# Performance work log

Hardware: AMD Instinct MI355X
Metric: run time of the kernel (lower is better)

Reference implementation:

```python
import jax, jax.numpy as jnp
import numpy as np

B, N, D, H = 4, 2048, 256, 8
d = D // H          # 32 per-head dim
EPS = 1e-5
SCALE = 1.0 / float(np.sqrt(d))


def setup_inputs() -> dict:
    key = jax.random.key(0)
    ks = jax.random.split(key, 6)
    s = 0.02
    x = jax.random.normal(ks[0], (B, N, D), jnp.float32)
    # RoPE frequencies: theta_j = 10000^(-2j/d), angle = pos * theta
    inv_freq = 1.0 / (10000.0 ** (jnp.arange(0, d, 2, dtype=jnp.float32) / d))  # (d/2,)
    ang = jnp.arange(N, dtype=jnp.float32)[:, None] * inv_freq[None, :]          # (N, d/2)
    return {
        "x": x,
        "freqs_cos": jnp.cos(ang),
        "freqs_sin": jnp.sin(ang),
        "w_qkv": jax.random.normal(ks[1], (D, 3 * D), jnp.float32) * s,
        "b_qkv": jnp.zeros((3 * D,), jnp.float32),
        "w_proj": jax.random.normal(ks[2], (D, D), jnp.float32) * s,
        "b_proj": jnp.zeros((D,), jnp.float32),
        "ln1_g": jnp.ones((D,), jnp.float32),
        "ln1_b": jnp.zeros((D,), jnp.float32),
        "ln2_g": jnp.ones((D,), jnp.float32),
        "ln2_b": jnp.zeros((D,), jnp.float32),
        "w1": jax.random.normal(ks[3], (D, 2 * D), jnp.float32) * s,
        "b1": jnp.zeros((2 * D,), jnp.float32),
        "w2": jax.random.normal(ks[4], (2 * D, D), jnp.float32) * s,
        "b2": jnp.zeros((D,), jnp.float32),
    }


def _layer_norm(x, g, b):
    mu = jnp.mean(x, axis=-1, keepdims=True)
    var = jnp.mean(jnp.square(x - mu), axis=-1, keepdims=True)
    return (x - mu) * jax.lax.rsqrt(var + EPS) * g + b


def _rope(t, cos, sin):
    # t: (B,H,N,d); interleaved (even,odd) pairs viewed as complex, multiplied by e^{i*ang}
    tr = t.reshape(B, H, N, d // 2, 2)
    te, to = tr[..., 0], tr[..., 1]
    c = cos[None, None, :, :]
    s = sin[None, None, :, :]
    oe = te * c - to * s
    oo = te * s + to * c
    return jnp.stack([oe, oo], axis=-1).reshape(B, H, N, d)


def reference(x, freqs_cos, freqs_sin, w_qkv, b_qkv, w_proj, b_proj,
              ln1_g, ln1_b, ln2_g, ln2_b, w1, b1, w2, b2):
    # Pre-LN MHSA with RoPE (dropout = identity at eval)
    h = _layer_norm(x, ln1_g, ln1_b)
    qkv = (h @ w_qkv + b_qkv).reshape(B, N, 3, H, d).transpose(0, 2, 3, 1, 4)  # (B,3,H,N,d)
    q, k, v = qkv[:, 0], qkv[:, 1], qkv[:, 2]
    q = _rope(q, freqs_cos, freqs_sin)
    k = _rope(k, freqs_cos, freqs_sin)
    attn = jax.nn.softmax(jnp.einsum('bhnd,bhmd->bhnm', q, k) * SCALE, axis=-1)
    out = jnp.einsum('bhnm,bhmd->bhnd', attn, v).transpose(0, 2, 1, 3).reshape(B, N, D)
    x = x + (out @ w_proj + b_proj)
    h = _layer_norm(x, ln2_g, ln2_b)
    ffn = jax.nn.relu(h @ w1 + b1) @ w2 + b2
    return x + ffn
```

## Files before the change

### kernel.cpp

```cpp
#include <hip/hip_runtime.h>
#include <hip/hip_bf16.h>
#include <math.h>

#define Bsz 4
#define Nseq 2048
#define Dm 256
#define Hh 8
#define Hd 32
#define EPS_ 1e-5f
#define SCALE_ 0.17677669529663687f
#define QSC_ (0.17677669529663687f * 1.4426950408889634f)

typedef __attribute__((ext_vector_type(8))) short short8;
typedef __attribute__((ext_vector_type(4))) short short4v;
typedef __attribute__((ext_vector_type(4))) float f32x4;
typedef __attribute__((ext_vector_type(16))) float f32x16;

__device__ __forceinline__ void gload16(const void* g, void* l) {
    __builtin_amdgcn_global_load_lds(
        (const __attribute__((address_space(1))) void*)g,
        (__attribute__((address_space(3))) void*)l, 16, 0, 0);
}

__device__ __forceinline__ short bf16s(float f) {
    __hip_bfloat16 h = __float2bfloat16(f);
    return *(short*)&h;
}

__device__ __forceinline__ int pkbf(float a, float b) {
    __hip_bfloat16 lo = __float2bfloat16(a), hi2 = __float2bfloat16(b);
    return (int)(((unsigned int)*(unsigned short*)&hi2 << 16) |
                 (unsigned int)*(unsigned short*)&lo);
}

union I4S8 { int i[4]; short8 s; };

__global__ __launch_bounds__(256) void ln_kernel(const float* __restrict__ x,
                                                 const float* __restrict__ g,
                                                 const float* __restrict__ b,
                                                 __hip_bfloat16* __restrict__ out) {
    int row  = blockIdx.x * 4 + (threadIdx.x >> 6);
    int lane = threadIdx.x & 63;
    const float* xr = x + (size_t)row * Dm;
    float4 v = *(const float4*)(xr + lane * 4);
    float s  = v.x + v.y + v.z + v.w;
    float ss = v.x * v.x + v.y * v.y + v.z * v.z + v.w * v.w;
    #pragma unroll
    for (int off = 32; off; off >>= 1) {
        s  += __shfl_xor(s, off);
        ss += __shfl_xor(ss, off);
    }
    float mu  = s * (1.0f / Dm);
    float var = ss * (1.0f / Dm) - mu * mu;
    float rs  = rsqrtf(var + EPS_);
    float4 gv = *(const float4*)(g + lane * 4);
    float4 bv = *(const float4*)(b + lane * 4);
    short4v o4 = { bf16s((v.x - mu) * rs * gv.x + bv.x),
                   bf16s((v.y - mu) * rs * gv.y + bv.y),
                   bf16s((v.z - mu) * rs * gv.z + bv.z),
                   bf16s((v.w - mu) * rs * gv.w + bv.w) };
    *(short4v*)(out + (size_t)row * Dm + lane * 4) = o4;
}

__global__ __launch_bounds__(256) void wconv_kernel(
    const float* __restrict__ s0, const float* __restrict__ s1,
    const float* __restrict__ s2, const float* __restrict__ s3,
    __hip_bfloat16* __restrict__ d0, __hip_bfloat16* __restrict__ d1,
    __hip_bfloat16* __restrict__ d2, __hip_bfloat16* __restrict__ d3) {
    __shared__ float t[32][33];
    int bid = blockIdx.x;
    const float* src; __hip_bfloat16* dst; int K, N, tb;
    if (bid < 192)      { src = s0; dst = d0; K = 256; N = 768; tb = bid; }
    else if (bid < 256) { src = s1; dst = d1; K = 256; N = 256; tb = bid - 192; }
    else if (bid < 384) { src = s2; dst = d2; K = 256; N = 512; tb = bid - 256; }
    else                { src = s3; dst = d3; K = 512; N = 256; tb = bid - 384; }
    int tn = N >> 5;
    int k0 = (tb / tn) * 32, n0 = (tb % tn) * 32;
    int c = threadIdx.x & 31, r0 = threadIdx.x >> 5;
    #pragma unroll
    for (int i = 0; i < 4; i++) {
        int r = r0 + i * 8;
        t[r][c] = src[(size_t)(k0 + r) * N + n0 + c];
    }
    __syncthreads();
    #pragma unroll
    for (int i = 0; i < 4; i++) {
        int n = r0 + i * 8;
        dst[(size_t)(n0 + n) * K + k0 + c] = __float2bfloat16(t[c][n]);
    }
}

template <int TM, int EPI>
__global__ __launch_bounds__(256) void mfma_gemm(const __hip_bfloat16* __restrict__ A,
                                                 const __hip_bfloat16* __restrict__ Wt,
                                                 const float* __restrict__ bias,
                                                 const float* __restrict__ res,
                                                 float* __restrict__ Cf,
                                                 __hip_bfloat16* __restrict__ Cb,
                                                 int M, int Nn, int K) {
    constexpr int MF = TM / 64;
    __shared__ __align__(16) __hip_bfloat16 As[TM * 32];
    __shared__ __align__(16) __hip_bfloat16 Bs[64 * 32];
    const int tid = threadIdx.x, w = tid >> 6, lane = tid & 63;
    const int lm = lane & 15, lq = lane >> 4;
    const int bm = blockIdx.y * TM, bn = blockIdx.x * 64;
    f32x4 acc[MF][4];
    #pragma unroll
    for (int i = 0; i < MF; i++)
        #pragma unroll
        for (int j = 0; j < 4; j++) acc[i][j] = (f32x4){0.f, 0.f, 0.f, 0.f};

    const int sw = (lq ^ (lm & 3)) * 8;
    for (int k0 = 0; k0 < K; k0 += 32) {
        #pragma unroll
        for (int p = 0; p < MF; p++) {
            int c = p * 256 + tid;
            int r = c >> 2, gk = ((c & 3) ^ (r & 3)) * 8;
            gload16(A + (size_t)(bm + r) * K + k0 + gk, As + (p * 256 + w * 64) * 8);
        }
        {
            int r = tid >> 2, gk = ((tid & 3) ^ (r & 3)) * 8;
            gload16(Wt + (size_t)(bn + r) * K + k0 + gk, Bs + w * 512);
        }
        __syncthreads();
        short8 a[MF];
        #pragma unroll
        for (int mf = 0; mf < MF; mf++)
            a[mf] = *(const short8*)&As[(w * (TM / 4) + mf * 16 + lm) * 32 + sw];
        #pragma unroll
        for (int nf = 0; nf < 4; nf++) {
            short8 bfr = *(const short8*)&Bs[(nf * 16 + lm) * 32 + sw];
            #pragma unroll
            for (int mf = 0; mf < MF; mf++)
                acc[mf][nf] = __builtin_amdgcn_mfma_f32_16x16x32_bf16(a[mf], bfr, acc[mf][nf], 0, 0, 0);
        }
        __syncthreads();
    }
    #pragma unroll
    for (int nf = 0; nf < 4; nf++) {
        int cg = bn + nf * 16 + lm;
        float bi = bias[cg];
        #pragma unroll
        for (int mf = 0; mf < MF; mf++) {
            #pragma unroll
            for (int r = 0; r < 4; r++) {
                int rg = bm + w * (TM / 4) + mf * 16 + lq * 4 + r;
                float v = acc[mf][nf][r] + bi;
                if (EPI == 1) {
                    v = fmaxf(v, 0.f);
                    Cb[(size_t)rg * Nn + cg] = __float2bfloat16(v);
                } else {
                    v += res[(size_t)rg * Nn + cg];
                    Cf[(size_t)rg * Nn + cg] = v;
                }
            }
        }
    }
}

__global__ __launch_bounds__(256) void qkv_mfma(const __hip_bfloat16* __restrict__ A,
                                                const __hip_bfloat16* __restrict__ Wt,
                                                const float* __restrict__ bias,
                                                const float* __restrict__ fcos,
                                                const float* __restrict__ fsin,
                                                __hip_bfloat16* __restrict__ qout,
                                                __hip_bfloat16* __restrict__ kout,
                                                __hip_bfloat16* __restrict__ vt) {
    const int K = 256, Nn = 768;
    __shared__ __align__(16) __hip_bfloat16 As[128 * 32];
    __shared__ __align__(16) __hip_bfloat16 Bs[64 * 32];
    const int tid = threadIdx.x, w = tid >> 6, lane = tid & 63;
    const int lm = lane & 15, lq = lane >> 4;
    const int bm = blockIdx.y * 128, bn = blockIdx.x * 64;
    f32x4 acc[2][4];
    #pragma unroll
    for (int i = 0; i < 2; i++)
        #pragma unroll
        for (int j = 0; j < 4; j++) acc[i][j] = (f32x4){0.f, 0.f, 0.f, 0.f};

    const int sw = (lq ^ (lm & 3)) * 8;
    for (int k0 = 0; k0 < K; k0 += 32) {
        #pragma unroll
        for (int p = 0; p < 2; p++) {
            int c = p * 256 + tid;
            int r = c >> 2, gk = ((c & 3) ^ (r & 3)) * 8;
            gload16(A + (size_t)(bm + r) * K + k0 + gk, As + (p * 256 + w * 64) * 8);
        }
        {
            int r = tid >> 2, gk = ((tid & 3) ^ (r & 3)) * 8;
            gload16(Wt + (size_t)(bn + r) * K + k0 + gk, Bs + w * 512);
        }
        __syncthreads();
        short8 a0 = *(const short8*)&As[(w * 32 + lm) * 32 + sw];
        short8 a1 = *(const short8*)&As[(w * 32 + 16 + lm) * 32 + sw];
        #pragma unroll
        for (int nf = 0; nf < 4; nf++) {
            short8 bfr = *(const short8*)&Bs[(nf * 16 + lm) * 32 + sw];
            acc[0][nf] = __builtin_amdgcn_mfma_f32_16x16x32_bf16(a0, bfr, acc[0][nf], 0, 0, 0);
            acc[1][nf] = __builtin_amdgcn_mfma_f32_16x16x32_bf16(a1, bfr, acc[1][nf], 0, 0, 0);
        }
        __syncthreads();
    }
    const int seg = bn >> 8;
    #pragma unroll
    for (int nf = 0; nf < 4; nf++) {
        int cg = bn + nf * 16 + lm;
        int hh = (cg & 255) >> 5;
        int dd = (nf & 1) * 16 + lm;
        int i0 = dd >> 1;
        float bi = bias[cg];
        #pragma unroll
        for (int mf = 0; mf < 2; mf++) {
            #pragma unroll
            for (int r = 0; r < 4; r++) {
                int rg = bm + w * 32 + mf * 16 + lq * 4 + r;
                int bb = rg >> 11, n = rg & (Nseq - 1);
                float v = acc[mf][nf][r] + bi;
                if (seg == 2) {
                    vt[(((size_t)(bb * Hh + hh)) * Hd + dd) * Nseq + n] = __float2bfloat16(v);
                } else {
                    float vp = __shfl_xor(v, 1);
                    float cs = fcos[n * 16 + i0], sn = fsin[n * 16 + i0];
                    float outv = (dd & 1) ? (vp * sn + v * cs) : (v * cs - vp * sn);
                    if (seg == 0) outv *= QSC_;
                    __hip_bfloat16* dst = (seg == 0) ? qout : kout;
                    dst[(((size_t)(bb * Hh + hh)) * Nseq + n) * Hd + dd] = __float2bfloat16(outv);
                }
            }
        }
    }
}

__global__ __launch_bounds__(256) void attn_mfma(const __hip_bfloat16* __restrict__ q,
                                                 const __hip_bfloat16* __restrict__ k,
                                                 const __hip_bfloat16* __restrict__ vt,
                                                 __hip_bfloat16* __restrict__ att) {
    __shared__ __align__(16) __hip_bfloat16 Qs[128 * 32];
    __shared__ __align__(16) __hip_bfloat16 Ks[2][32 * 64];
    __shared__ __align__(16) __hip_bfloat16 Vs[2][32 * 64];
    __shared__ float smS[4][32];
    const int tid = threadIdx.x, w = tid >> 6;
    const int lane = tid & 63, l31 = lane & 31, hi = lane >> 5;
    const int bh = blockIdx.y, qbase = blockIdx.x * 128;
    const __hip_bfloat16* qp = q + ((size_t)bh * Nseq + qbase) * Hd;
    const __hip_bfloat16* kp = k + (size_t)bh * Nseq * Hd;
    const __hip_bfloat16* vp = vt + (size_t)bh * Hd * Nseq;

    const int r8 = tid >> 3, s8 = tid & 7;
    #pragma unroll
    for (int p = 0; p < 2; p++) {
        int c = p * 256 + tid, r = c >> 2, sl = c & 3;
        gload16(qp + r * 32 + ((sl ^ (r & 3)) * 8), Qs + (p * 256 + w * 64) * 8);
    }
    gload16(kp + (2 * r8 + (s8 >> 2)) * 32 + (((s8 & 3) ^ (r8 & 3)) * 8), Ks[0] + w * 512);
    gload16(vp + (size_t)r8 * Nseq + ((s8 ^ (r8 & 7)) * 8), Vs[0] + w * 512);
    __syncthreads();

    const int qrow = w * 32 + l31;
    short8 qf0 = *(const short8*)&Qs[qrow * 32 + ((hi ^ (l31 & 3)) * 8)];
    short8 qf1 = *(const short8*)&Qs[qrow * 32 + (((2 + hi) ^ (l31 & 3)) * 8)];

    f32x16 O;
    #pragma unroll
    for (int i = 0; i < 16; i++) O[i] = 0.f;
    float sm = 0.f;

    for (int kt = 0; kt < Nseq / 64; kt++) {
        const int cur = kt & 1;
        if (kt + 1 < Nseq / 64) {
            gload16(kp + ((kt + 1) * 64 + 2 * r8 + (s8 >> 2)) * 32 + (((s8 & 3) ^ (r8 & 3)) * 8),
                    Ks[cur ^ 1] + w * 512);
            gload16(vp + (size_t)r8 * Nseq + (kt + 1) * 64 + ((s8 ^ (r8 & 7)) * 8),
                    Vs[cur ^ 1] + w * 512);
        }
        f32x16 St0, St1;
        #pragma unroll
        for (int i = 0; i < 16; i++) { St0[i] = 0.f; St1[i] = 0.f; }
        {
            int prow = l31 >> 1;
            int elb = prow * 64 + (l31 & 1) * 32;
            short8 kf0 = *(const short8*)&Ks[cur][elb + ((hi ^ (prow & 3)) * 8)];
            short8 kf1 = *(const short8*)&Ks[cur][elb + (((2 + hi) ^ (prow & 3)) * 8)];
            St0 = __builtin_amdgcn_mfma_f32_32x32x16_bf16(kf0, qf0, St0, 0, 0, 0);
            St0 = __builtin_amdgcn_mfma_f32_32x32x16_bf16(kf1, qf1, St0, 0, 0, 0);
        }
        {
            int prow = 16 + (l31 >> 1);
            int elb = prow * 64 + (l31 & 1) * 32;
            short8 kf0 = *(const short8*)&Ks[cur][elb + ((hi ^ (prow & 3)) * 8)];
            short8 kf1 = *(const short8*)&Ks[cur][elb + (((2 + hi) ^ (prow & 3)) * 8)];
            St1 = __builtin_amdgcn_mfma_f32_32x32x16_bf16(kf0, qf0, St1, 0, 0, 0);
            St1 = __builtin_amdgcn_mfma_f32_32x32x16_bf16(kf1, qf1, St1, 0, 0, 0);
        }
        int pk0[8], pk1[8];
        #pragma unroll
        for (int p = 0; p < 8; p++) {
            float a = exp2f(St0[2 * p]), b = exp2f(St0[2 * p + 1]);
            sm += a + b;
            pk0[p] = pkbf(a, b);
        }
        #pragma unroll
        for (int p = 0; p < 8; p++) {
            float a = exp2f(St1[2 * p]), b = exp2f(St1[2 * p + 1]);
            sm += a + b;
            pk1[p] = pkbf(a, b);
        }
        #pragma unroll
        for (int t = 0; t < 4; t++) {
            const int* PK = (t >> 1) ? pk1 : pk0;
            const int base = 4 * (t & 1);
            int keep0 = hi ? PK[base + 2] : PK[base + 0];
            int keep1 = hi ? PK[base + 3] : PK[base + 1];
            int send0 = hi ? PK[base + 0] : PK[base + 2];
            int send1 = hi ? PK[base + 1] : PK[base + 3];
            int x0 = __shfl_xor(send0, 32);
            int x1 = __shfl_xor(send1, 32);
            I4S8 u;
            u.i[0] = hi ? x0 : keep0;
            u.i[1] = hi ? x1 : keep1;
            u.i[2] = hi ? keep0 : x0;
            u.i[3] = hi ? keep1 : x1;
            short8 vf = *(const short8*)&Vs[cur][l31 * 64 + (((2 * t + hi) ^ (l31 & 7)) * 8)];
            O = __builtin_amdgcn_mfma_f32_32x32x16_bf16(u.s, vf, O, 0, 0, 0);
        }
        __syncthreads();
    }
    sm += __shfl_xor(sm, 32);
    if (hi == 0) smS[w][l31] = sm;
    __syncthreads();
    const int bb = bh >> 3, hh = bh & 7;
    #pragma unroll
    for (int m = 0; m < 4; m++) {
        float4 sv = *(const float4*)&smS[w][8 * m + 4 * hi];
        #pragma unroll
        for (int i = 0; i < 4; i++) {
            int n = qbase + w * 32 + 8 * m + 4 * hi + i;
            att[((size_t)(bb * Nseq + n)) * Dm + hh * Hd + l31] =
                __float2bfloat16(O[4 * m + i] * (1.0f / sv[i]));
        }
    }
}

extern "C" void kernel_launch(void* const* d_in, const int* in_sizes, int n_in,
                              void* d_out, int out_size, void* d_ws, size_t ws_size,
                              hipStream_t stream) {
    const float* x      = (const float*)d_in[0];
    const float* fcos   = (const float*)d_in[1];
    const float* fsin   = (const float*)d_in[2];
    const float* w_qkv  = (const float*)d_in[3];
    const float* b_qkv  = (const float*)d_in[4];
    const float* w_proj = (const float*)d_in[5];
    const float* b_proj = (const float*)d_in[6];
    const float* ln1_g  = (const float*)d_in[7];
    const float* ln1_b  = (const float*)d_in[8];
    const float* ln2_g  = (const float*)d_in[9];
    const float* ln2_b  = (const float*)d_in[10];
    const float* w1     = (const float*)d_in[11];
    const float* b1     = (const float*)d_in[12];
    const float* w2     = (const float*)d_in[13];
    const float* b2     = (const float*)d_in[14];
    float* out = (float*)d_out;
    char* base = (char*)d_ws;
    const size_t MB = (size_t)1 << 20;

    __hip_bfloat16* h   = (__hip_bfloat16*)(base);
    __hip_bfloat16* qb  = (__hip_bfloat16*)(base + 4 * MB);
    __hip_bfloat16* kbf = (__hip_bfloat16*)(base + 8 * MB);
    __hip_bfloat16* vtb = (__hip_bfloat16*)(base + 12 * MB);
    __hip_bfloat16* att = (__hip_bfloat16*)(base + 16 * MB);
    float*          x2f = (float*)(base + 20 * MB);
    __hip_bfloat16* h2  = (__hip_bfloat16*)(base);
    __hip_bfloat16* ffn = (__hip_bfloat16*)(base + 28 * MB);
    __hip_bfloat16* wqT = (__hip_bfloat16*)(base + 40 * MB);
    __hip_bfloat16* wpT = (__hip_bfloat16*)(base + 40 * MB + 393216);
    __hip_bfloat16* w1T = (__hip_bfloat16*)(base + 40 * MB + 524288);
    __hip_bfloat16* w2T = (__hip_bfloat16*)(base + 40 * MB + 786432);

    const int rows = Bsz * Nseq;

    wconv_kernel<<<512, 256, 0, stream>>>(w_qkv, w_proj, w1, w2, wqT, wpT, w1T, w2T);
    ln_kernel<<<rows / 4, 256, 0, stream>>>(x, ln1_g, ln1_b, h);
    qkv_mfma<<<dim3(12, 64), 256, 0, stream>>>(h, wqT, b_qkv, fcos, fsin, qb, kbf, vtb);
    attn_mfma<<<dim3(Nseq / 128, Bsz * Hh), 256, 0, stream>>>(qb, kbf, vtb, att);
    mfma_gemm<64, 2><<<dim3(4, 128), 256, 0, stream>>>(att, wpT, b_proj, x, x2f, nullptr,
                                                       rows, 256, 256);
    ln_kernel<<<rows / 4, 256, 0, stream>>>(x2f, ln2_g, ln2_b, h2);
    mfma_gemm<128, 1><<<dim3(8, 64), 256, 0, stream>>>(h2, w1T, b1, nullptr, nullptr, ffn,
                                                       rows, 512, 256);
    mfma_gemm<64, 2><<<dim3(4, 128), 256, 0, stream>>>(ffn, w2T, b2, x2f, out, nullptr,
                                                       rows, 256, 512);
}
```

Before: 205.0 us.

## Split attention key range across wave pairs and cheapen exp/bf16 packing

Result: faster. 184.5 us (-10.0%).

```diff
diff --git a/kernel.cpp b/kernel.cpp
--- a/kernel.cpp
+++ b/kernel.cpp
@@ -27,10 +27,11 @@
     return *(short*)&h;
 }
 
-__device__ __forceinline__ int pkbf(float a, float b) {
-    __hip_bfloat16 lo = __float2bfloat16(a), hi2 = __float2bfloat16(b);
-    return (int)(((unsigned int)*(unsigned short*)&hi2 << 16) |
-                 (unsigned int)*(unsigned short*)&lo);
+union FU { float f; unsigned u; };
+
+__device__ __forceinline__ int pk2bf(float a, float b) {
+    FU ua, ub; ua.f = a; ub.f = b;
+    return (int)__builtin_amdgcn_perm(ub.u, ua.u, 0x07060302u);
 }
 
 union I4S8 { int i[4]; short8 s; };
@@ -235,28 +236,37 @@
                                                  const __hip_bfloat16* __restrict__ k,
                                                  const __hip_bfloat16* __restrict__ vt,
                                                  __hip_bfloat16* __restrict__ att) {
-    __shared__ __align__(16) __hip_bfloat16 Qs[128 * 32];
-    __shared__ __align__(16) __hip_bfloat16 Ks[2][32 * 64];
-    __shared__ __align__(16) __hip_bfloat16 Vs[2][32 * 64];
-    __shared__ float smS[4][32];
-    const int tid = threadIdx.x, w = tid >> 6;
-    const int lane = tid & 63, l31 = lane & 31, hi = lane >> 5;
-    const int bh = blockIdx.y, qbase = blockIdx.x * 128;
+    __shared__ __align__(16) char smem[4096 + 16384 + 16384 + 512];
+    __hip_bfloat16* Qs  = (__hip_bfloat16*)smem;
+    __hip_bfloat16* KsB = (__hip_bfloat16*)(smem + 4096);
+    __hip_bfloat16* VsB = (__hip_bfloat16*)(smem + 20480);
+    float* RedO = (float*)(smem + 4096);
+    float* RedS = (float*)(smem + 4096 + 8192);
+    float* smS  = (float*)(smem + 4096 + 8192 + 256);
+
+    const int tid = threadIdx.x, w = tid >> 6, lane = tid & 63;
+    const int l31 = lane & 31, hi = lane >> 5;
+    const int wq = w >> 1, wk = w & 1;
+    const int bh = blockIdx.y, qbase = blockIdx.x * 64;
     const __hip_bfloat16* qp = q + ((size_t)bh * Nseq + qbase) * Hd;
     const __hip_bfloat16* kp = k + (size_t)bh * Nseq * Hd;
     const __hip_bfloat16* vp = vt + (size_t)bh * Hd * Nseq;
-
     const int r8 = tid >> 3, s8 = tid & 7;
-    #pragma unroll
-    for (int p = 0; p < 2; p++) {
-        int c = p * 256 + tid, r = c >> 2, sl = c & 3;
-        gload16(qp + r * 32 + ((sl ^ (r & 3)) * 8), Qs + (p * 256 + w * 64) * 8);
-    }
-    gload16(kp + (2 * r8 + (s8 >> 2)) * 32 + (((s8 & 3) ^ (r8 & 3)) * 8), Ks[0] + w * 512);
-    gload16(vp + (size_t)r8 * Nseq + ((s8 ^ (r8 & 7)) * 8), Vs[0] + w * 512);
+
+    {
+        int r = tid >> 2, sl = tid & 3;
+        gload16(qp + r * 32 + ((sl ^ (r & 3)) * 8), Qs + w * 512);
+    }
+    #pragma unroll
+    for (int par = 0; par < 2; par++) {
+        gload16(kp + (par * 64 + 2 * r8 + (s8 >> 2)) * 32 + (((s8 & 3) ^ (r8 & 3)) * 8),
+                KsB + par * 2048 + w * 512);
+        gload16(vp + (size_t)r8 * Nseq + par * 64 + ((s8 ^ (r8 & 7)) * 8),
+                VsB + par * 2048 + w * 512);
+    }
     __syncthreads();
 
-    const int qrow = w * 32 + l31;
+    const int qrow = wq * 32 + l31;
     short8 qf0 = *(const short8*)&Qs[qrow * 32 + ((hi ^ (l31 & 3)) * 8)];
     short8 qf1 = *(const short8*)&Qs[qrow * 32 + (((2 + hi) ^ (l31 & 3)) * 8)];
 
@@ -265,50 +275,56 @@
     for (int i = 0; i < 16; i++) O[i] = 0.f;
     float sm = 0.f;
 
-    for (int kt = 0; kt < Nseq / 64; kt++) {
-        const int cur = kt & 1;
-        if (kt + 1 < Nseq / 64) {
-            gload16(kp + ((kt + 1) * 64 + 2 * r8 + (s8 >> 2)) * 32 + (((s8 & 3) ^ (r8 & 3)) * 8),
-                    Ks[cur ^ 1] + w * 512);
-            gload16(vp + (size_t)r8 * Nseq + (kt + 1) * 64 + ((s8 ^ (r8 & 7)) * 8),
-                    Vs[cur ^ 1] + w * 512);
-        }
+    for (int t = 0; t < 16; t++) {
+        const int buf = t & 1;
+        if (t + 1 < 16) {
+            const int kb2 = (t + 1) * 128;
+            #pragma unroll
+            for (int par = 0; par < 2; par++) {
+                gload16(kp + (kb2 + par * 64 + 2 * r8 + (s8 >> 2)) * 32 + (((s8 & 3) ^ (r8 & 3)) * 8),
+                        KsB + ((buf ^ 1) * 2 + par) * 2048 + w * 512);
+                gload16(vp + (size_t)r8 * Nseq + kb2 + par * 64 + ((s8 ^ (r8 & 7)) * 8),
+                        VsB + ((buf ^ 1) * 2 + par) * 2048 + w * 512);
+            }
+        }
+        const __hip_bfloat16* Kc = KsB + (buf * 2 + wk) * 2048;
+        const __hip_bfloat16* Vc = VsB + (buf * 2 + wk) * 2048;
         f32x16 St0, St1;
         #pragma unroll
         for (int i = 0; i < 16; i++) { St0[i] = 0.f; St1[i] = 0.f; }
         {
-            int prow = l31 >> 1;
-            int elb = prow * 64 + (l31 & 1) * 32;
-            short8 kf0 = *(const short8*)&Ks[cur][elb + ((hi ^ (prow & 3)) * 8)];
-            short8 kf1 = *(const short8*)&Ks[cur][elb + (((2 + hi) ^ (prow & 3)) * 8)];
+            int pr = l31 >> 1, elb = pr * 64 + (l31 & 1) * 32;
+            short8 kf0 = *(const short8*)&Kc[elb + ((hi ^ (pr & 3)) * 8)];
+            short8 kf1 = *(const short8*)&Kc[elb + (((2 + hi) ^ (pr & 3)) * 8)];
             St0 = __builtin_amdgcn_mfma_f32_32x32x16_bf16(kf0, qf0, St0, 0, 0, 0);
             St0 = __builtin_amdgcn_mfma_f32_32x32x16_bf16(kf1, qf1, St0, 0, 0, 0);
         }
         {
-            int prow = 16 + (l31 >> 1);
-            int elb = prow * 64 + (l31 & 1) * 32;
-            short8 kf0 = *(const short8*)&Ks[cur][elb + ((hi ^ (prow & 3)) * 8)];
-            short8 kf1 = *(const short8*)&Ks[cur][elb + (((2 + hi) ^ (prow & 3)) * 8)];
+            int pr = 16 + (l31 >> 1), elb = pr * 64 + (l31 & 1) * 32;
+            short8 kf0 = *(const short8*)&Kc[elb + ((hi ^ (pr & 3)) * 8)];
+            short8 kf1 = *(const short8*)&Kc[elb + (((2 + hi) ^ (pr & 3)) * 8)];
             St1 = __builtin_amdgcn_mfma_f32_32x32x16_bf16(kf0, qf0, St1, 0, 0, 0);
             St1 = __builtin_amdgcn_mfma_f32_32x32x16_bf16(kf1, qf1, St1, 0, 0, 0);
         }
         int pk0[8], pk1[8];
         #pragma unroll
         for (int p = 0; p < 8; p++) {
-            float a = exp2f(St0[2 * p]), b = exp2f(St0[2 * p + 1]);
+            float a = __builtin_amdgcn_exp2f(St0[2 * p]);
+            float b = __builtin_amdgcn_exp2f(St0[2 * p + 1]);
             sm += a + b;
-            pk0[p] = pkbf(a, b);
+            pk0[p] = pk2bf(a, b);
         }
         #pragma unroll
         for (int p = 0; p < 8; p++) {
-            float a = exp2f(St1[2 * p]), b = exp2f(St1[2 * p + 1]);
+            float a = __builtin_amdgcn_exp2f(St1[2 * p]);
+            float b = __builtin_amdgcn_exp2f(St1[2 * p + 1]);
             sm += a + b;
-            pk1[p] = pkbf(a, b);
-        }
-        #pragma unroll
-        for (int t = 0; t < 4; t++) {
-            const int* PK = (t >> 1) ? pk1 : pk0;
-            const int base = 4 * (t & 1);
+            pk1[p] = pk2bf(a, b);
+        }
+        #pragma unroll
+        for (int tt = 0; tt < 4; tt++) {
+            const int* PK = (tt >> 1) ? pk1 : pk0;
+            const int base = 4 * (tt & 1);
             int keep0 = hi ? PK[base + 2] : PK[base + 0];
             int keep1 = hi ? PK[base + 3] : PK[base + 1];
             int send0 = hi ? PK[base + 0] : PK[base + 2];
@@ -320,23 +336,36 @@
             u.i[1] = hi ? x1 : keep1;
             u.i[2] = hi ? keep0 : x0;
             u.i[3] = hi ? keep1 : x1;
-            short8 vf = *(const short8*)&Vs[cur][l31 * 64 + (((2 * t + hi) ^ (l31 & 7)) * 8)];
+            short8 vf = *(const short8*)&Vc[l31 * 64 + (((2 * tt + hi) ^ (l31 & 7)) * 8)];
             O = __builtin_amdgcn_mfma_f32_32x32x16_bf16(u.s, vf, O, 0, 0, 0);
         }
         __syncthreads();
     }
     sm += __shfl_xor(sm, 32);
-    if (hi == 0) smS[w][l31] = sm;
+    if (wk == 1) {
+        #pragma unroll
+        for (int j = 0; j < 16; j++) RedO[(wq * 16 + j) * 64 + lane] = O[j];
+        if (hi == 0) RedS[wq * 32 + l31] = sm;
+    }
     __syncthreads();
-    const int bb = bh >> 3, hh = bh & 7;
-    #pragma unroll
-    for (int m = 0; m < 4; m++) {
-        float4 sv = *(const float4*)&smS[w][8 * m + 4 * hi];
-        #pragma unroll
-        for (int i = 0; i < 4; i++) {
-            int n = qbase + w * 32 + 8 * m + 4 * hi + i;
-            att[((size_t)(bb * Nseq + n)) * Dm + hh * Hd + l31] =
-                __float2bfloat16(O[4 * m + i] * (1.0f / sv[i]));
+    if (wk == 0) {
+        #pragma unroll
+        for (int j = 0; j < 16; j++) O[j] += RedO[(wq * 16 + j) * 64 + lane];
+        sm += RedS[wq * 32 + l31];
+        if (hi == 0) smS[wq * 32 + l31] = sm;
+    }
+    __syncthreads();
+    if (wk == 0) {
+        const int bb = bh >> 3, hh = bh & 7;
+        #pragma unroll
+        for (int m = 0; m < 4; m++) {
+            float4 sv = *(const float4*)&smS[wq * 32 + 8 * m + 4 * hi];
+            #pragma unroll
+            for (int i = 0; i < 4; i++) {
+                int n = qbase + wq * 32 + 8 * m + 4 * hi + i;
+                att[((size_t)(bb * Nseq + n)) * Dm + hh * Hd + l31] =
+                    __float2bfloat16(O[4 * m + i] * (1.0f / sv[i]));
+            }
         }
     }
 }
@@ -381,7 +410,7 @@
     wconv_kernel<<<512, 256, 0, stream>>>(w_qkv, w_proj, w1, w2, wqT, wpT, w1T, w2T);
     ln_kernel<<<rows / 4, 256, 0, stream>>>(x, ln1_g, ln1_b, h);
     qkv_mfma<<<dim3(12, 64), 256, 0, stream>>>(h, wqT, b_qkv, fcos, fsin, qb, kbf, vtb);
-    attn_mfma<<<dim3(Nseq / 128, Bsz * Hh), 256, 0, stream>>>(qb, kbf, vtb, att);
+    attn_mfma<<<dim3(Nseq / 64, Bsz * Hh), 256, 0, stream>>>(qb, kbf, vtb, att);
     mfma_gemm<64, 2><<<dim3(4, 128), 256, 0, stream>>>(att, wpT, b_proj, x, x2f, nullptr,
                                                        rows, 256, 256);
     ln_kernel<<<rows / 4, 256, 0, stream>>>(x2f, ln2_g, ln2_b, h2);
```
